# Optimization experiments

Hardware: AMD Instinct MI355X
Metric: run time of the kernel (lower is better)

Reference implementation:

```python
import jax, jax.numpy as jnp
import numpy as np

N_NODES = 20000
N_EDGES = 640000
D = 128
H = 256


def setup_inputs() -> dict:
    key = jax.random.key(0)
    ks = jax.random.split(key, 8)
    s = lambda fan_in: 1.0 / np.sqrt(fan_in)
    return {
        "nf": jax.random.normal(ks[0], (N_NODES, D), jnp.float32),
        "ef": jax.random.normal(ks[1], (N_EDGES, D), jnp.float32),
        "src": jax.random.randint(ks[2], (N_EDGES,), 0, N_NODES, jnp.int32),
        "dst": jax.random.randint(ks[3], (N_EDGES,), 0, N_NODES, jnp.int32),
        "We1": jax.random.normal(ks[4], (3 * D, H), jnp.float32) * s(3 * D),
        "be1": jnp.zeros((H,), jnp.float32),
        "We2": jax.random.normal(ks[5], (H, D), jnp.float32) * s(H),
        "be2": jnp.zeros((D,), jnp.float32),
        "Wn1": jax.random.normal(ks[6], (2 * D, H), jnp.float32) * s(2 * D),
        "bn1": jnp.zeros((H,), jnp.float32),
        "Wn2": jax.random.normal(ks[7], (H, D), jnp.float32) * s(H),
        "bn2": jnp.zeros((D,), jnp.float32),
    }


def reference(nf, ef, src, dst, We1, be1, We2, be2, Wn1, bn1, Wn2, bn2):
    # edge update: concat [ef, sender_nf, receiver_nf] -> MLP
    em_in = jnp.concatenate([ef, nf[src], nf[dst]], axis=-1)  # [E, 3D]
    h = jax.nn.relu(em_in @ We1 + be1)
    updated_ef = h @ We2 + be2  # [E, D]
    # message = copy_e('h'); aggregate = segment sum at destination nodes
    agg_m = jax.ops.segment_sum(updated_ef, dst, num_segments=nf.shape[0])  # [N, D]
    # node update: concat [agg_m, nf] -> MLP
    nm_in = jnp.concatenate([agg_m, nf], axis=-1)  # [N, 2D]
    hn = jax.nn.relu(nm_in @ Wn1 + bn1)
    updated_nf = hn @ Wn2 + bn2  # [N, D]
    return updated_nf, updated_ef
```

## Files before the change

kernel.cpp:

```cpp
#include <hip/hip_runtime.h>
#include <hip/hip_bf16.h>

#define N_NODES 20000
#define N_EDGES 640000
#define D 128
#define H 256

using bf16x8 = __attribute__((ext_vector_type(8))) short;
using f32x4  = __attribute__((ext_vector_type(4))) float;

__device__ __forceinline__ unsigned short f2bf(float f) {
  unsigned int u = __float_as_uint(f);
  unsigned int r = u + 0x7fffu + ((u >> 16) & 1u);
  return (unsigned short)(r >> 16);
}

__global__ __launch_bounds__(256) void prep_kernel(
    const float* __restrict__ nf,
    const float* __restrict__ We1, const float* __restrict__ We2,
    const float* __restrict__ Wn1, const float* __restrict__ Wn2,
    float* __restrict__ agg, unsigned short* __restrict__ nf_bf,
    unsigned short* __restrict__ We1T, unsigned short* __restrict__ We2T,
    unsigned short* __restrict__ Wn1T, unsigned short* __restrict__ Wn2T) {
  int idx = blockIdx.x * 256 + threadIdx.x;
  if (idx < N_NODES * D) {
    agg[idx] = 0.f;
    nf_bf[idx] = f2bf(nf[idx]);
  }
  if (idx < 98304) {
    int n = idx / 384, k = idx % 384;
    We1T[idx] = f2bf(We1[k * 256 + n]);
  } else if (idx < 98304 + 32768) {
    int j = idx - 98304; int n = j / 256, k = j % 256;
    We2T[j] = f2bf(We2[k * 128 + n]);
  } else if (idx < 98304 + 32768 + 65536) {
    int j = idx - 131072; int n = j / 256, k = j % 256;
    Wn1T[j] = f2bf(Wn1[k * 256 + n]);
  } else if (idx < 229376) {
    int j = idx - 196608; int n = j / 256, k = j % 256;
    Wn2T[j] = f2bf(Wn2[k * 128 + n]);
  }
}

#define AS 392
#define HS 264

__global__ __launch_bounds__(256, 3) void edge_kernel(
    const float* __restrict__ ef, const unsigned short* __restrict__ nf_bf,
    const int* __restrict__ src, const int* __restrict__ dst,
    const unsigned short* __restrict__ We1T, const float* __restrict__ be1,
    const unsigned short* __restrict__ We2T, const float* __restrict__ be2,
    float* __restrict__ out_ef, float* __restrict__ agg) {
  __shared__ unsigned short smem[64 * AS];
  unsigned short* hbuf = smem;

  const int tid  = threadIdx.x;
  const int lane = tid & 63;
  const int wave = tid >> 6;
  const int ln15 = lane & 15;
  const int q    = lane >> 4;
  const int e0   = blockIdx.x * 64;

  {
    const float4* ef4 = (const float4*)ef;
#pragma unroll
    for (int i = 0; i < 8; i++) {
      int flat = tid + 256 * i;
      int row = flat >> 5, c4 = flat & 31;
      float4 v = ef4[(size_t)(e0 + row) * 32 + c4];
      ushort4 o = { f2bf(v.x), f2bf(v.y), f2bf(v.z), f2bf(v.w) };
      *(ushort4*)&smem[row * AS + c4 * 4] = o;
    }
#pragma unroll
    for (int i = 0; i < 4; i++) {
      int flat = tid + 256 * i;
      int row = flat >> 4, seg = flat & 15;
      int e = e0 + row;
      int s = src[e];
      int d = dst[e];
      *(uint4*)&smem[row * AS + 128 + seg * 8] =
          *(const uint4*)&nf_bf[(size_t)s * 128 + seg * 8];
      *(uint4*)&smem[row * AS + 256 + seg * 8] =
          *(const uint4*)&nf_bf[(size_t)d * 128 + seg * 8];
    }
  }
  __syncthreads();

  const int nb1 = wave * 64;
  f32x4 acc[4][4] = {};
  float bias1[4];
#pragma unroll
  for (int nt = 0; nt < 4; nt++) bias1[nt] = be1[nb1 + nt * 16 + ln15];

#pragma unroll
  for (int ks = 0; ks < 12; ks++) {
    const int kc = ks * 32 + q * 8;
    bf16x8 a[4], b[4];
#pragma unroll
    for (int mt = 0; mt < 4; mt++)
      a[mt] = *(const bf16x8*)&smem[(mt * 16 + ln15) * AS + kc];
#pragma unroll
    for (int nt = 0; nt < 4; nt++)
      b[nt] = *(const bf16x8*)&We1T[(size_t)(nb1 + nt * 16 + ln15) * 384 + kc];
#pragma unroll
    for (int mt = 0; mt < 4; mt++)
#pragma unroll
      for (int nt = 0; nt < 4; nt++)
        acc[mt][nt] = __builtin_amdgcn_mfma_f32_16x16x32_bf16(a[mt], b[nt], acc[mt][nt], 0, 0, 0);
  }
  __syncthreads();

#pragma unroll
  for (int mt = 0; mt < 4; mt++)
#pragma unroll
    for (int nt = 0; nt < 4; nt++)
#pragma unroll
      for (int r = 0; r < 4; r++) {
        float v = acc[mt][nt][r] + bias1[nt];
        v = v > 0.f ? v : 0.f;
        hbuf[(mt * 16 + q * 4 + r) * HS + nb1 + nt * 16 + ln15] = f2bf(v);
      }
  __syncthreads();

  const int nb2 = wave * 32;
  f32x4 acc2[4][2] = {};
  float bias2[2];
#pragma unroll
  for (int nt = 0; nt < 2; nt++) bias2[nt] = be2[nb2 + nt * 16 + ln15];

#pragma unroll
  for (int ks = 0; ks < 8; ks++) {
    const int kc = ks * 32 + q * 8;
    bf16x8 a2[4], b2[2];
#pragma unroll
    for (int mt = 0; mt < 4; mt++)
      a2[mt] = *(const bf16x8*)&hbuf[(mt * 16 + ln15) * HS + kc];
#pragma unroll
    for (int nt = 0; nt < 2; nt++)
      b2[nt] = *(const bf16x8*)&We2T[(size_t)(nb2 + nt * 16 + ln15) * 256 + kc];
#pragma unroll
    for (int mt = 0; mt < 4; mt++)
#pragma unroll
      for (int nt = 0; nt < 2; nt++)
        acc2[mt][nt] = __builtin_amdgcn_mfma_f32_16x16x32_bf16(a2[mt], b2[nt], acc2[mt][nt], 0, 0, 0);
  }

#pragma unroll
  for (int mt = 0; mt < 4; mt++) {
#pragma unroll
    for (int r = 0; r < 4; r++) {
      int row = mt * 16 + q * 4 + r;
      int e = e0 + row;
      int d = dst[e];
#pragma unroll
      for (int nt = 0; nt < 2; nt++) {
        int col = nb2 + nt * 16 + ln15;
        float v = acc2[mt][nt][r] + bias2[nt];
        out_ef[(size_t)e * 128 + col] = v;
        atomicAdd(&agg[(size_t)d * 128 + col], v);
      }
    }
  }
}

__global__ __launch_bounds__(256, 3) void node_kernel(
    const float* __restrict__ agg, const unsigned short* __restrict__ nf_bf,
    const unsigned short* __restrict__ Wn1T, const float* __restrict__ bn1,
    const unsigned short* __restrict__ Wn2T, const float* __restrict__ bn2,
    float* __restrict__ out_nf) {
  __shared__ unsigned short smem[64 * HS];

  const int tid  = threadIdx.x;
  const int lane = tid & 63;
  const int wave = tid >> 6;
  const int ln15 = lane & 15;
  const int q    = lane >> 4;
  const int n0   = blockIdx.x * 64;

  {
    const float4* agg4 = (const float4*)agg;
#pragma unroll
    for (int i = 0; i < 8; i++) {
      int flat = tid + 256 * i;
      int row = flat >> 5, c4 = flat & 31;
      int node = n0 + row;
      float4 v = make_float4(0.f, 0.f, 0.f, 0.f);
      if (node < N_NODES) v = agg4[(size_t)node * 32 + c4];
      ushort4 o = { f2bf(v.x), f2bf(v.y), f2bf(v.z), f2bf(v.w) };
      *(ushort4*)&smem[row * HS + c4 * 4] = o;
    }
#pragma unroll
    for (int i = 0; i < 4; i++) {
      int flat = tid + 256 * i;
      int row = flat >> 4, seg = flat & 15;
      int node = n0 + row;
      uint4 v = make_uint4(0u, 0u, 0u, 0u);
      if (node < N_NODES) v = *(const uint4*)&nf_bf[(size_t)node * 128 + seg * 8];
      *(uint4*)&smem[row * HS + 128 + seg * 8] = v;
    }
  }
  __syncthreads();

  const int nb1 = wave * 64;
  f32x4 acc[4][4] = {};
  float bias1[4];
#pragma unroll
  for (int nt = 0; nt < 4; nt++) bias1[nt] = bn1[nb1 + nt * 16 + ln15];

#pragma unroll
  for (int ks = 0; ks < 8; ks++) {
    const int kc = ks * 32 + q * 8;
    bf16x8 a[4], b[4];
#pragma unroll
    for (int mt = 0; mt < 4; mt++)
      a[mt] = *(const bf16x8*)&smem[(mt * 16 + ln15) * HS + kc];
#pragma unroll
    for (int nt = 0; nt < 4; nt++)
      b[nt] = *(const bf16x8*)&Wn1T[(size_t)(nb1 + nt * 16 + ln15) * 256 + kc];
#pragma unroll
    for (int mt = 0; mt < 4; mt++)
#pragma unroll
      for (int nt = 0; nt < 4; nt++)
        acc[mt][nt] = __builtin_amdgcn_mfma_f32_16x16x32_bf16(a[mt], b[nt], acc[mt][nt], 0, 0, 0);
  }
  __syncthreads();

#pragma unroll
  for (int mt = 0; mt < 4; mt++)
#pragma unroll
    for (int nt = 0; nt < 4; nt++)
#pragma unroll
      for (int r = 0; r < 4; r++) {
        float v = acc[mt][nt][r] + bias1[nt];
        v = v > 0.f ? v : 0.f;
        smem[(mt * 16 + q * 4 + r) * HS + nb1 + nt * 16 + ln15] = f2bf(v);
      }
  __syncthreads();

  const int nb2 = wave * 32;
  f32x4 acc2[4][2] = {};
  float bias2[2];
#pragma unroll
  for (int nt = 0; nt < 2; nt++) bias2[nt] = bn2[nb2 + nt * 16 + ln15];

#pragma unroll
  for (int ks = 0; ks < 8; ks++) {
    const int kc = ks * 32 + q * 8;
    bf16x8 a2[4], b2[2];
#pragma unroll
    for (int mt = 0; mt < 4; mt++)
      a2[mt] = *(const bf16x8*)&smem[(mt * 16 + ln15) * HS + kc];
#pragma unroll
    for (int nt = 0; nt < 2; nt++)
      b2[nt] = *(const bf16x8*)&Wn2T[(size_t)(nb2 + nt * 16 + ln15) * 256 + kc];
#pragma unroll
    for (int mt = 0; mt < 4; mt++)
#pragma unroll
      for (int nt = 0; nt < 2; nt++)
        acc2[mt][nt] = __builtin_amdgcn_mfma_f32_16x16x32_bf16(a2[mt], b2[nt], acc2[mt][nt], 0, 0, 0);
  }

#pragma unroll
  for (int mt = 0; mt < 4; mt++) {
#pragma unroll
    for (int r = 0; r < 4; r++) {
      int row = mt * 16 + q * 4 + r;
      int node = n0 + row;
      if (node < N_NODES) {
#pragma unroll
        for (int nt = 0; nt < 2; nt++) {
          int col = nb2 + nt * 16 + ln15;
          out_nf[(size_t)node * 128 + col] = acc2[mt][nt][r] + bias2[nt];
        }
      }
    }
  }
}

extern "C" void kernel_launch(void* const* d_in, const int* in_sizes, int n_in,
                              void* d_out, int out_size, void* d_ws, size_t ws_size,
                              hipStream_t stream) {
  const float* nf  = (const float*)d_in[0];
  const float* ef  = (const float*)d_in[1];
  const int*   src = (const int*)d_in[2];
  const int*   dst = (const int*)d_in[3];
  const float* We1 = (const float*)d_in[4];
  const float* be1 = (const float*)d_in[5];
  const float* We2 = (const float*)d_in[6];
  const float* be2 = (const float*)d_in[7];
  const float* Wn1 = (const float*)d_in[8];
  const float* bn1 = (const float*)d_in[9];
  const float* Wn2 = (const float*)d_in[10];
  const float* bn2 = (const float*)d_in[11];

  float* out_nf = (float*)d_out;
  float* out_ef = out_nf + (size_t)N_NODES * D;

  char* ws = (char*)d_ws;
  float*          agg   = (float*)ws;
  unsigned short* nf_bf = (unsigned short*)(ws + 10240000);
  unsigned short* We1T  = (unsigned short*)(ws + 15360000);
  unsigned short* We2T  = (unsigned short*)(ws + 15556608);
  unsigned short* Wn1T  = (unsigned short*)(ws + 15622144);
  unsigned short* Wn2T  = (unsigned short*)(ws + 15753216);

  prep_kernel<<<10000, 256, 0, stream>>>(nf, We1, We2, Wn1, Wn2,
                                         agg, nf_bf, We1T, We2T, Wn1T, Wn2T);
  edge_kernel<<<N_EDGES / 64, 256, 0, stream>>>(ef, nf_bf, src, dst,
                                                We1T, be1, We2T, be2, out_ef, agg);
  node_kernel<<<(N_NODES + 63) / 64, 256, 0, stream>>>(agg, nf_bf,
                                                       Wn1T, bn1, Wn2T, bn2, out_nf);
}
```

Before: 1.010 ms.

## Replace per-edge float atomics with CSR gather-based segment sum in node kernel

```diff
diff --git a/kernel.cpp b/kernel.cpp
--- a/kernel.cpp
+++ b/kernel.cpp
@@ -16,16 +16,18 @@
 }
 
 __global__ __launch_bounds__(256) void prep_kernel(
-    const float* __restrict__ nf,
+    const float* __restrict__ nf, const int* __restrict__ dst,
     const float* __restrict__ We1, const float* __restrict__ We2,
     const float* __restrict__ Wn1, const float* __restrict__ Wn2,
-    float* __restrict__ agg, unsigned short* __restrict__ nf_bf,
-    unsigned short* __restrict__ We1T, unsigned short* __restrict__ We2T,
-    unsigned short* __restrict__ Wn1T, unsigned short* __restrict__ Wn2T) {
+    unsigned short* __restrict__ nf_bf, unsigned short* __restrict__ We1T,
+    unsigned short* __restrict__ We2T, unsigned short* __restrict__ Wn1T,
+    unsigned short* __restrict__ Wn2T, int* __restrict__ deg) {
   int idx = blockIdx.x * 256 + threadIdx.x;
   if (idx < N_NODES * D) {
-    agg[idx] = 0.f;
     nf_bf[idx] = f2bf(nf[idx]);
+  }
+  if (idx < N_EDGES) {
+    atomicAdd(&deg[dst[idx]], 1);
   }
   if (idx < 98304) {
     int n = idx / 384, k = idx % 384;
@@ -42,6 +44,47 @@
   }
 }
 
+__global__ __launch_bounds__(1024) void scan_kernel(const int* __restrict__ deg,
+                                                    int* __restrict__ cursor) {
+  __shared__ int sums[1024];
+  const int t = threadIdx.x;
+  const int base = t * 20;
+  int local[20];
+  int s = 0;
+#pragma unroll
+  for (int i = 0; i < 20; i++) {
+    int p = base + i;
+    int v = (p < N_NODES) ? deg[p] : 0;
+    local[i] = s;
+    s += v;
+  }
+  sums[t] = s;
+  __syncthreads();
+  for (int ofs = 1; ofs < 1024; ofs <<= 1) {
+    int v = (t >= ofs) ? sums[t - ofs] : 0;
+    __syncthreads();
+    sums[t] += v;
+    __syncthreads();
+  }
+  int ebase = sums[t] - s;
+#pragma unroll
+  for (int i = 0; i < 20; i++) {
+    int p = base + i;
+    if (p < N_NODES) cursor[p] = ebase + local[i];
+  }
+}
+
+__global__ __launch_bounds__(256) void fill_kernel(const int* __restrict__ dst,
+                                                   int* __restrict__ cursor,
+                                                   int* __restrict__ eidx) {
+  int e = blockIdx.x * 256 + threadIdx.x;
+  if (e < N_EDGES) {
+    int d = dst[e];
+    int pos = atomicAdd(&cursor[d], 1);
+    eidx[pos] = e;
+  }
+}
+
 #define AS 392
 #define HS 264
 
@@ -50,7 +93,7 @@
     const int* __restrict__ src, const int* __restrict__ dst,
     const unsigned short* __restrict__ We1T, const float* __restrict__ be1,
     const unsigned short* __restrict__ We2T, const float* __restrict__ be2,
-    float* __restrict__ out_ef, float* __restrict__ agg) {
+    float* __restrict__ out_ef) {
   __shared__ unsigned short smem[64 * AS];
   unsigned short* hbuf = smem;
 
@@ -151,20 +194,18 @@
     for (int r = 0; r < 4; r++) {
       int row = mt * 16 + q * 4 + r;
       int e = e0 + row;
-      int d = dst[e];
 #pragma unroll
       for (int nt = 0; nt < 2; nt++) {
         int col = nb2 + nt * 16 + ln15;
-        float v = acc2[mt][nt][r] + bias2[nt];
-        out_ef[(size_t)e * 128 + col] = v;
-        atomicAdd(&agg[(size_t)d * 128 + col], v);
+        out_ef[(size_t)e * 128 + col] = acc2[mt][nt][r] + bias2[nt];
       }
     }
   }
 }
 
 __global__ __launch_bounds__(256, 3) void node_kernel(
-    const float* __restrict__ agg, const unsigned short* __restrict__ nf_bf,
+    const float* __restrict__ out_ef, const unsigned short* __restrict__ nf_bf,
+    const int* __restrict__ cursor, const int* __restrict__ eidx,
     const unsigned short* __restrict__ Wn1T, const float* __restrict__ bn1,
     const unsigned short* __restrict__ Wn2T, const float* __restrict__ bn2,
     float* __restrict__ out_nf) {
@@ -178,17 +219,41 @@
   const int n0   = blockIdx.x * 64;
 
   {
-    const float4* agg4 = (const float4*)agg;
-#pragma unroll
-    for (int i = 0; i < 8; i++) {
-      int flat = tid + 256 * i;
-      int row = flat >> 5, c4 = flat & 31;
+    const float2* ef2 = (const float2*)out_ef;
+    for (int nl = 0; nl < 16; ++nl) {
+      int row  = wave * 16 + nl;
       int node = n0 + row;
-      float4 v = make_float4(0.f, 0.f, 0.f, 0.f);
-      if (node < N_NODES) v = agg4[(size_t)node * 32 + c4];
-      ushort4 o = { f2bf(v.x), f2bf(v.y), f2bf(v.z), f2bf(v.w) };
-      *(ushort4*)&smem[row * HS + c4 * 4] = o;
-    }
+      float a0x=0.f,a0y=0.f,a1x=0.f,a1y=0.f,a2x=0.f,a2y=0.f,a3x=0.f,a3y=0.f;
+      if (node < N_NODES) {
+        int s = (node == 0) ? 0 : cursor[node - 1];
+        int t = cursor[node];
+        int j = s;
+        for (; j + 8 <= t; j += 8) {
+          int e0v=eidx[j],   e1v=eidx[j+1], e2v=eidx[j+2], e3v=eidx[j+3];
+          int e4v=eidx[j+4], e5v=eidx[j+5], e6v=eidx[j+6], e7v=eidx[j+7];
+          float2 v0=ef2[(size_t)e0v*64+lane], v1=ef2[(size_t)e1v*64+lane];
+          float2 v2=ef2[(size_t)e2v*64+lane], v3=ef2[(size_t)e3v*64+lane];
+          float2 v4=ef2[(size_t)e4v*64+lane], v5=ef2[(size_t)e5v*64+lane];
+          float2 v6=ef2[(size_t)e6v*64+lane], v7=ef2[(size_t)e7v*64+lane];
+          a0x+=v0.x+v4.x; a0y+=v0.y+v4.y;
+          a1x+=v1.x+v5.x; a1y+=v1.y+v5.y;
+          a2x+=v2.x+v6.x; a2y+=v2.y+v6.y;
+          a3x+=v3.x+v7.x; a3y+=v3.y+v7.y;
+        }
+        for (; j < t; ++j) {
+          int ev = eidx[j];
+          float2 v = ef2[(size_t)ev*64+lane];
+          a0x += v.x; a0y += v.y;
+        }
+      }
+      float ax = (a0x + a1x) + (a2x + a3x);
+      float ay = (a0y + a1y) + (a2y + a3y);
+      unsigned int packed = (unsigned int)f2bf(ax) | ((unsigned int)f2bf(ay) << 16);
+      *(unsigned int*)&smem[row * HS + 2 * lane] = packed;
+    }
+  }
+
+  {
 #pragma unroll
     for (int i = 0; i < 4; i++) {
       int flat = tid + 256 * i;
@@ -297,17 +362,22 @@
   float* out_ef = out_nf + (size_t)N_NODES * D;
 
   char* ws = (char*)d_ws;
-  float*          agg   = (float*)ws;
-  unsigned short* nf_bf = (unsigned short*)(ws + 10240000);
-  unsigned short* We1T  = (unsigned short*)(ws + 15360000);
-  unsigned short* We2T  = (unsigned short*)(ws + 15556608);
-  unsigned short* Wn1T  = (unsigned short*)(ws + 15622144);
-  unsigned short* Wn2T  = (unsigned short*)(ws + 15753216);
-
-  prep_kernel<<<10000, 256, 0, stream>>>(nf, We1, We2, Wn1, Wn2,
-                                         agg, nf_bf, We1T, We2T, Wn1T, Wn2T);
+  unsigned short* nf_bf = (unsigned short*)ws;
+  unsigned short* We1T  = (unsigned short*)(ws + 5120000);
+  unsigned short* We2T  = (unsigned short*)(ws + 5316608);
+  unsigned short* Wn1T  = (unsigned short*)(ws + 5382144);
+  unsigned short* Wn2T  = (unsigned short*)(ws + 5513216);
+  int*            deg   = (int*)(ws + 5578752);
+  int*            cursor= (int*)(ws + 5658752);
+  int*            eidx  = (int*)(ws + 5738752);
+
+  hipMemsetAsync(deg, 0, N_NODES * sizeof(int), stream);
+  prep_kernel<<<10000, 256, 0, stream>>>(nf, dst, We1, We2, Wn1, Wn2,
+                                         nf_bf, We1T, We2T, Wn1T, Wn2T, deg);
+  scan_kernel<<<1, 1024, 0, stream>>>(deg, cursor);
+  fill_kernel<<<N_EDGES / 256, 256, 0, stream>>>(dst, cursor, eidx);
   edge_kernel<<<N_EDGES / 64, 256, 0, stream>>>(ef, nf_bf, src, dst,
-                                                We1T, be1, We2T, be2, out_ef, agg);
-  node_kernel<<<(N_NODES + 63) / 64, 256, 0, stream>>>(agg, nf_bf,
+                                                We1T, be1, We2T, be2, out_ef);
+  node_kernel<<<(N_NODES + 63) / 64, 256, 0, stream>>>(out_ef, nf_bf, cursor, eidx,
                                                        Wn1T, bn1, Wn2T, bn2, out_nf);
 }
```

After: 1.099 ms. 8.8% more time.
